# Kernel tuning notes

Hardware: AMD Instinct MI355X
Metric: run time of the kernel (lower is better)

## Reference

```python
import jax, jax.numpy as jnp
import numpy as np

N = 100000   # nodes
E = 400000   # edges (avg degree 4, NoC-mesh-like)
H = 512      # hidden_channels
F_IN = 1     # num_node_features


def _lin(key, fan_in, fan_out):
    # torch.nn.Linear default init: U(-1/sqrt(fan_in), 1/sqrt(fan_in))
    bound = 1.0 / np.sqrt(fan_in)
    return jax.random.uniform(key, (fan_in, fan_out), jnp.float32, -bound, bound)


def setup_inputs() -> dict:
    key = jax.random.key(0)
    ks = jax.random.split(key, 16)
    inp = {
        "x": jax.random.normal(ks[0], (N, F_IN), jnp.float32),
        "edge_index": jax.random.randint(ks[1], (2, E), 0, N, jnp.int32),
        # conv1: in=1 -> out=512
        "w_rel1": _lin(ks[2], F_IN, H),
        "b_rel1": jax.random.uniform(ks[3], (H,), jnp.float32, -1.0, 1.0),
        "w_root1": _lin(ks[4], F_IN, H),
        # conv2..4: 512 -> 512
        "w_rel2": _lin(ks[5], H, H),
        "b_rel2": jax.random.uniform(ks[6], (H,), jnp.float32, -1/np.sqrt(H), 1/np.sqrt(H)),
        "w_root2": _lin(ks[7], H, H),
        "w_rel3": _lin(ks[8], H, H),
        "b_rel3": jax.random.uniform(ks[9], (H,), jnp.float32, -1/np.sqrt(H), 1/np.sqrt(H)),
        "w_root3": _lin(ks[10], H, H),
        "w_rel4": _lin(ks[11], H, H),
        "b_rel4": jax.random.uniform(ks[12], (H,), jnp.float32, -1/np.sqrt(H), 1/np.sqrt(H)),
        "w_root4": _lin(ks[13], H, H),
    }
    return inp


def _graph_conv(x, src, dst, w_rel, b_rel, w_root):
    # PyG GraphConv (aggr='add'): out_i = W_rel @ sum_{j in N(i)} x_j + b_rel + W_root @ x_i
    # messages flow src (edge_index[0]) -> dst (edge_index[1])
    agg = jax.ops.segment_sum(x[src], dst, num_segments=N)  # [N, F_in]
    return agg @ w_rel + b_rel + x @ w_root


def reference(x, edge_index,
              w_rel1, b_rel1, w_root1,
              w_rel2, b_rel2, w_root2,
              w_rel3, b_rel3, w_root3,
              w_rel4, b_rel4, w_root4):
    src, dst = edge_index[0], edge_index[1]
    x1 = jax.nn.relu(_graph_conv(x,  src, dst, w_rel1, b_rel1, w_root1))
    x2 = jax.nn.relu(_graph_conv(x1, src, dst, w_rel2, b_rel2, w_root2)) + x1
    x3 = _graph_conv(x2, src, dst, w_rel3, b_rel3, w_root3) + x2
    x4 = _graph_conv(x3, src, dst, w_rel4, b_rel4, w_root4) + x3
    return x4
```

## Files before the change

kernel.cpp:

```cpp
#include <hip/hip_runtime.h>

#define NN 100000
#define EE 400000
#define HH 512
#define NB_SCAN 98

typedef __attribute__((ext_vector_type(8))) short short8;
typedef __attribute__((ext_vector_type(8))) unsigned short ushort8;
typedef __attribute__((ext_vector_type(4))) float f32x4;

__device__ inline unsigned short f2b(float f) {
    unsigned int u = __float_as_uint(f);
    return (unsigned short)((u + 0x7fffu + ((u >> 16) & 1u)) >> 16);
}
__device__ inline float b2f(unsigned short b) {
    return __uint_as_float(((unsigned int)b) << 16);
}

__global__ void histo_deg(const int* __restrict__ dst, int* __restrict__ deg) {
    int e = blockIdx.x * blockDim.x + threadIdx.x;
    if (e < EE) atomicAdd(&deg[dst[e]], 1);
}

__global__ void scan_reduce(const int* __restrict__ deg, int* __restrict__ blockSums) {
    __shared__ int s[256];
    int b = blockIdx.x, t = threadIdx.x;
    int base = b * 1024 + t * 4;
    int v = 0;
    #pragma unroll
    for (int j = 0; j < 4; ++j) { int i = base + j; if (i < NN) v += deg[i]; }
    s[t] = v; __syncthreads();
    for (int off = 128; off > 0; off >>= 1) {
        if (t < off) s[t] += s[t + off];
        __syncthreads();
    }
    if (t == 0) blockSums[b] = s[0];
}

__global__ void scan_top(int* __restrict__ blockSums, int* __restrict__ start) {
    __shared__ int s[128];
    int t = threadIdx.x;
    s[t] = (t < NB_SCAN) ? blockSums[t] : 0;
    __syncthreads();
    for (int off = 1; off < 128; off <<= 1) {
        int u = (t >= off) ? s[t - off] : 0;
        __syncthreads();
        s[t] += u;
        __syncthreads();
    }
    if (t < NB_SCAN) blockSums[t] = (t == 0) ? 0 : s[t - 1];
    if (t == 0) start[NN] = EE;
}

__global__ void scan_down(const int* __restrict__ deg, const int* __restrict__ blockSums,
                          int* __restrict__ start, int* __restrict__ cursor) {
    __shared__ int s[256];
    int b = blockIdx.x, t = threadIdx.x;
    int base = b * 1024 + t * 4;
    int v[4]; int sum = 0;
    #pragma unroll
    for (int j = 0; j < 4; ++j) {
        int i = base + j;
        v[j] = (i < NN) ? deg[i] : 0;
        sum += v[j];
    }
    s[t] = sum; __syncthreads();
    for (int off = 1; off < 256; off <<= 1) {
        int u = (t >= off) ? s[t - off] : 0;
        __syncthreads();
        s[t] += u;
        __syncthreads();
    }
    int excl = blockSums[b] + ((t == 0) ? 0 : s[t - 1]);
    #pragma unroll
    for (int j = 0; j < 4; ++j) {
        int i = base + j;
        if (i < NN) { start[i] = excl; cursor[i] = excl; excl += v[j]; }
    }
}

__global__ void csr_fill(const int* __restrict__ src, const int* __restrict__ dst,
                         int* __restrict__ cursor, int* __restrict__ eidx) {
    int e = blockIdx.x * blockDim.x + threadIdx.x;
    if (e < EE) {
        int p = atomicAdd(&cursor[dst[e]], 1);
        eidx[p] = src[e];
    }
}

__global__ void w_transpose(const float* __restrict__ w, unsigned short* __restrict__ wt) {
    int idx = blockIdx.x * 256 + threadIdx.x;
    int n = idx >> 9, k = idx & 511;
    wt[idx] = f2b(w[(size_t)k * HH + n]);
}

__global__ __launch_bounds__(256) void gather_rows_b(
    const unsigned short* __restrict__ xb, const int* __restrict__ start,
    const int* __restrict__ eidx, unsigned short* __restrict__ agg)
{
    int node = blockIdx.x * 4 + (threadIdx.x >> 6);
    if (node >= NN) return;
    int c0 = (threadIdx.x & 63) << 3;
    float a[8] = {0.f,0.f,0.f,0.f,0.f,0.f,0.f,0.f};
    int e0 = start[node], e1 = start[node + 1];
    int e = e0;
    for (; e + 4 <= e1; e += 4) {
        int s0 = eidx[e], s1 = eidx[e + 1], s2 = eidx[e + 2], s3 = eidx[e + 3];
        ushort8 v0 = *(const ushort8*)(xb + (size_t)s0 * HH + c0);
        ushort8 v1 = *(const ushort8*)(xb + (size_t)s1 * HH + c0);
        ushort8 v2 = *(const ushort8*)(xb + (size_t)s2 * HH + c0);
        ushort8 v3 = *(const ushort8*)(xb + (size_t)s3 * HH + c0);
        #pragma unroll
        for (int j = 0; j < 8; ++j)
            a[j] += (b2f(v0[j]) + b2f(v1[j])) + (b2f(v2[j]) + b2f(v3[j]));
    }
    for (; e < e1; ++e) {
        ushort8 v = *(const ushort8*)(xb + (size_t)eidx[e] * HH + c0);
        #pragma unroll
        for (int j = 0; j < 8; ++j) a[j] += b2f(v[j]);
    }
    ushort8 o;
    #pragma unroll
    for (int j = 0; j < 8; ++j) o[j] = f2b(a[j]);
    *(ushort8*)(agg + (size_t)node * HH + c0) = o;
}

__global__ void gather_scalar(const float* __restrict__ x, const int* __restrict__ start,
                              const int* __restrict__ eidx, float* __restrict__ agg0) {
    int i = blockIdx.x * blockDim.x + threadIdx.x;
    if (i >= NN) return;
    float s = 0.f;
    int e1 = start[i + 1];
    for (int e = start[i]; e < e1; ++e) s += x[eidx[e]];
    agg0[i] = s;
}

__global__ void layer1_expand(const float* __restrict__ x,
                              const float* __restrict__ agg0,
                              const float* __restrict__ w_rel,
                              const float* __restrict__ b,
                              const float* __restrict__ w_root,
                              unsigned short* __restrict__ x1b) {
    int idx = blockIdx.x * blockDim.x + threadIdx.x;
    int i = idx >> 7;
    if (i >= NN) return;
    int q = (idx & 127) << 2;
    float a = agg0[i], xv = x[i];
    float4 wr = *(const float4*)&w_rel[q];
    float4 bb = *(const float4*)&b[q];
    float4 wt = *(const float4*)&w_root[q];
    float4 o;
    o.x = fmaxf(fmaf(a, wr.x, fmaf(xv, wt.x, bb.x)), 0.f);
    o.y = fmaxf(fmaf(a, wr.y, fmaf(xv, wt.y, bb.y)), 0.f);
    o.z = fmaxf(fmaf(a, wr.z, fmaf(xv, wt.z, bb.z)), 0.f);
    o.w = fmaxf(fmaf(a, wr.w, fmaf(xv, wt.w, bb.w)), 0.f);
    ushort4 ob = { f2b(o.x), f2b(o.y), f2b(o.z), f2b(o.w) };
    *(ushort4*)&x1b[(size_t)i * HH + q] = ob;
}

__device__ inline void gload16(const void* g, void* l) {
    __builtin_amdgcn_global_load_lds(
        (const __attribute__((address_space(1))) unsigned int*)g,
        (__attribute__((address_space(3))) unsigned int*)l,
        16, 0, 0);
}

template<bool RELU, bool F32OUT>
__global__ __launch_bounds__(256, 4) void gemm_mfma(
    const unsigned short* __restrict__ AB, const unsigned short* __restrict__ XBp,
    const unsigned short* __restrict__ WrT, const unsigned short* __restrict__ WoT,
    const float* __restrict__ bias, const unsigned short* __restrict__ residb,
    float* __restrict__ out, unsigned short* __restrict__ outb)
{
    __shared__ unsigned short As[2 * 128 * 32];
    __shared__ unsigned short Bs[2 * 128 * 32];
    const int tid  = threadIdx.x;
    const int wave = tid >> 6, lane = tid & 63;

    const int bid = blockIdx.x;
    const int nid = (bid & 7) * 391 + (bid >> 3);
    const int col0 = (nid & 3) << 7;
    const int row0 = (nid >> 2) << 7;

    const int wr = wave >> 1, wc = wave & 1;
    const int l16 = lane & 15, lq = lane >> 4;
    const int sRow = lane >> 2;
    const int sColSwz = (((lane & 3) ^ ((lane >> 3) & 3)) << 3);
    const int xorslot = ((lq ^ ((lane >> 1) & 3)) << 3);

    int rowA[2], colB[2];
    #pragma unroll
    for (int i = 0; i < 2; ++i) {
        int chunk = (wave << 1) + i;
        int gr = row0 + chunk * 16 + sRow;
        rowA[i] = (gr >= NN) ? (NN - 1) : gr;
        colB[i] = col0 + chunk * 16 + sRow;
    }

    f32x4 acc[4][4];
    #pragma unroll
    for (int m = 0; m < 4; ++m)
        #pragma unroll
        for (int n = 0; n < 4; ++n)
            acc[m][n] = (f32x4){0.f, 0.f, 0.f, 0.f};

    auto STAGE = [&](unsigned short* Asb, unsigned short* Bsb, int t) {
        const int k0 = t << 5;
        const unsigned short* Ap = (k0 < 512) ? AB  : XBp;
        const unsigned short* Wp = (k0 < 512) ? WrT : WoT;
        const int kk = k0 & 511;
        #pragma unroll
        for (int i = 0; i < 2; ++i) {
            int chunk = (wave << 1) + i;
            gload16(Ap + (size_t)rowA[i] * HH + kk + sColSwz, Asb + chunk * 512);
            gload16(Wp + (size_t)colB[i] * HH + kk + sColSwz, Bsb + chunk * 512);
        }
    };

    auto COMPUTE = [&](const unsigned short* Asb, const unsigned short* Bsb) {
        short8 af[4], bfv[4];
        #pragma unroll
        for (int m = 0; m < 4; ++m)
            af[m] = *(const short8*)(Asb + (wr * 64 + m * 16 + l16) * 32 + xorslot);
        #pragma unroll
        for (int n = 0; n < 4; ++n)
            bfv[n] = *(const short8*)(Bsb + (wc * 64 + n * 16 + l16) * 32 + xorslot);
        #pragma unroll
        for (int m = 0; m < 4; ++m)
            #pragma unroll
            for (int n = 0; n < 4; ++n)
                acc[m][n] = __builtin_amdgcn_mfma_f32_16x16x32_bf16(af[m], bfv[n], acc[m][n], 0, 0, 0);
    };

    unsigned short* A0 = As;        unsigned short* A1 = As + 4096;
    unsigned short* B0 = Bs;        unsigned short* B1 = Bs + 4096;

    STAGE(A0, B0, 0);
    __syncthreads();
    #pragma unroll 1
    for (int t = 0; t < 32; t += 2) {
        STAGE(A1, B1, t + 1);
        COMPUTE(A0, B0);
        __syncthreads();
        if (t + 2 < 32) STAGE(A0, B0, t + 2);
        COMPUTE(A1, B1);
        __syncthreads();
    }

    float bias_n[4];
    #pragma unroll
    for (int n = 0; n < 4; ++n) bias_n[n] = bias[col0 + wc * 64 + n * 16 + l16];

    #pragma unroll
    for (int m = 0; m < 4; ++m) {
        #pragma unroll
        for (int j = 0; j < 4; ++j) {
            int row = row0 + wr * 64 + m * 16 + lq * 4 + j;
            if (row >= NN) continue;
            #pragma unroll
            for (int n = 0; n < 4; ++n) {
                int col = col0 + wc * 64 + n * 16 + l16;
                size_t off = (size_t)row * HH + col;
                float v = acc[m][n][j] + bias_n[n];
                if (RELU) v = fmaxf(v, 0.f);
                v += b2f(residb[off]);
                if (F32OUT) out[off] = v;
                else        outb[off] = f2b(v);
            }
        }
    }
}

extern "C" void kernel_launch(void* const* d_in, const int* in_sizes, int n_in,
                              void* d_out, int out_size, void* d_ws, size_t ws_size,
                              hipStream_t stream) {
    const float* x   = (const float*)d_in[0];
    const int*   ei  = (const int*)d_in[1];
    const int*   src = ei;
    const int*   dst = ei + EE;
    const float* w_rel1  = (const float*)d_in[2];
    const float* b_rel1  = (const float*)d_in[3];
    const float* w_root1 = (const float*)d_in[4];
    const float* w_rel2  = (const float*)d_in[5];
    const float* b_rel2  = (const float*)d_in[6];
    const float* w_root2 = (const float*)d_in[7];
    const float* w_rel3  = (const float*)d_in[8];
    const float* b_rel3  = (const float*)d_in[9];
    const float* w_root3 = (const float*)d_in[10];
    const float* w_rel4  = (const float*)d_in[11];
    const float* b_rel4  = (const float*)d_in[12];
    const float* w_root4 = (const float*)d_in[13];

    const size_t NH = (size_t)NN * HH;
    unsigned short* XB   = (unsigned short*)d_ws;
    unsigned short* XB2  = XB + NH;
    unsigned short* X3B  = XB2 + NH;
    unsigned short* AGB  = X3B + NH;
    unsigned short* WT   = AGB + NH;
    float*          agg0 = (float*)(WT + 6 * 262144);
    int*            csr  = (int*)(agg0 + NN);
    int* deg       = csr;
    int* start     = csr + NN;
    int* cursor    = start + NN + 1;
    int* eidx      = cursor + NN;
    int* blockSums = eidx + EE;
    float* out = (float*)d_out;

    unsigned short* WrT2 = WT;
    unsigned short* WoT2 = WT + 1 * 262144;
    unsigned short* WrT3 = WT + 2 * 262144;
    unsigned short* WoT3 = WT + 3 * 262144;
    unsigned short* WrT4 = WT + 4 * 262144;
    unsigned short* WoT4 = WT + 5 * 262144;

    const int gGemm = 3128;

    hipMemsetAsync(deg, 0, NN * sizeof(int), stream);
    histo_deg<<<(EE + 255) / 256, 256, 0, stream>>>(dst, deg);
    scan_reduce<<<NB_SCAN, 256, 0, stream>>>(deg, blockSums);
    scan_top<<<1, 128, 0, stream>>>(blockSums, start);
    scan_down<<<NB_SCAN, 256, 0, stream>>>(deg, blockSums, start, cursor);
    csr_fill<<<(EE + 255) / 256, 256, 0, stream>>>(src, dst, cursor, eidx);

    w_transpose<<<1024, 256, 0, stream>>>(w_rel2,  WrT2);
    w_transpose<<<1024, 256, 0, stream>>>(w_root2, WoT2);
    w_transpose<<<1024, 256, 0, stream>>>(w_rel3,  WrT3);
    w_transpose<<<1024, 256, 0, stream>>>(w_root3, WoT3);
    w_transpose<<<1024, 256, 0, stream>>>(w_rel4,  WrT4);
    w_transpose<<<1024, 256, 0, stream>>>(w_root4, WoT4);

    gather_scalar<<<(NN + 255) / 256, 256, 0, stream>>>(x, start, eidx, agg0);
    layer1_expand<<<50000, 256, 0, stream>>>(x, agg0, w_rel1, b_rel1, w_root1, XB);

    gather_rows_b<<<25000, 256, 0, stream>>>(XB, start, eidx, AGB);
    gemm_mfma<true, false><<<gGemm, 256, 0, stream>>>(
        AGB, XB, WrT2, WoT2, b_rel2, XB, nullptr, XB2);

    gather_rows_b<<<25000, 256, 0, stream>>>(XB2, start, eidx, AGB);
    gemm_mfma<false, false><<<gGemm, 256, 0, stream>>>(
        AGB, XB2, WrT3, WoT3, b_rel3, XB2, nullptr, X3B);

    gather_rows_b<<<25000, 256, 0, stream>>>(X3B, start, eidx, AGB);
    gemm_mfma<false, true><<<gGemm, 256, 0, stream>>>(
        AGB, X3B, WrT4, WoT4, b_rel4, X3B, out, nullptr);
}
```

Measured before the change: 810.6 us.

## Fold linear layers 3 and 4 into one GEMM via precomputed weight products

```diff
diff --git a/kernel.cpp b/kernel.cpp
--- a/kernel.cpp
+++ b/kernel.cpp
@@ -88,10 +88,31 @@
     }
 }
 
-__global__ void w_transpose(const float* __restrict__ w, unsigned short* __restrict__ wt) {
+__global__ void w_transpose(const float* __restrict__ w, unsigned short* __restrict__ wt, int addI) {
     int idx = blockIdx.x * 256 + threadIdx.x;
     int n = idx >> 9, k = idx & 511;
-    wt[idx] = f2b(w[(size_t)k * HH + n]);
+    float v = w[(size_t)k * HH + n] + ((addI && k == n) ? 1.f : 0.f);
+    wt[idx] = f2b(v);
+}
+__global__ void w_convert(const float* __restrict__ w, unsigned short* __restrict__ wb, int addI) {
+    int idx = blockIdx.x * 256 + threadIdx.x;
+    int k = idx >> 9, j = idx & 511;
+    float v = w[idx] + ((addI && k == j) ? 1.f : 0.f);
+    wb[idx] = f2b(v);
+}
+__global__ void cvec(const float* __restrict__ b3, const float* __restrict__ Wr4,
+                     const float* __restrict__ Wo4, const float* __restrict__ b4,
+                     float* __restrict__ c1, float* __restrict__ c2) {
+    int n = blockIdx.x * 256 + threadIdx.x;
+    if (n >= HH) return;
+    float a1 = 0.f, a2 = 0.f;
+    for (int j = 0; j < HH; ++j) {
+        float bj = b3[j];
+        a1 = fmaf(bj, Wr4[(size_t)j * HH + n], a1);
+        a2 = fmaf(bj, Wo4[(size_t)j * HH + n], a2);
+    }
+    c1[n] = a1;
+    c2[n] = a2 + b3[n] + b4[n];
 }
 
 __global__ __launch_bounds__(256) void gather_rows_b(
@@ -165,23 +186,20 @@
         16, 0, 0);
 }
 
-template<bool RELU, bool F32OUT>
-__global__ __launch_bounds__(256, 4) void gemm_mfma(
+__global__ __launch_bounds__(256, 3) void gemm_l2(
     const unsigned short* __restrict__ AB, const unsigned short* __restrict__ XBp,
     const unsigned short* __restrict__ WrT, const unsigned short* __restrict__ WoT,
     const float* __restrict__ bias, const unsigned short* __restrict__ residb,
-    float* __restrict__ out, unsigned short* __restrict__ outb)
+    unsigned short* __restrict__ outb)
 {
     __shared__ unsigned short As[2 * 128 * 32];
     __shared__ unsigned short Bs[2 * 128 * 32];
     const int tid  = threadIdx.x;
     const int wave = tid >> 6, lane = tid & 63;
-
     const int bid = blockIdx.x;
     const int nid = (bid & 7) * 391 + (bid >> 3);
     const int col0 = (nid & 3) << 7;
     const int row0 = (nid >> 2) << 7;
-
     const int wr = wave >> 1, wc = wave & 1;
     const int l16 = lane & 15, lq = lane >> 4;
     const int sRow = lane >> 2;
@@ -201,8 +219,7 @@
     #pragma unroll
     for (int m = 0; m < 4; ++m)
         #pragma unroll
-        for (int n = 0; n < 4; ++n)
-            acc[m][n] = (f32x4){0.f, 0.f, 0.f, 0.f};
+        for (int n = 0; n < 4; ++n) acc[m][n] = (f32x4){0.f,0.f,0.f,0.f};
 
     auto STAGE = [&](unsigned short* Asb, unsigned short* Bsb, int t) {
         const int k0 = t << 5;
@@ -216,7 +233,6 @@
             gload16(Wp + (size_t)colB[i] * HH + kk + sColSwz, Bsb + chunk * 512);
         }
     };
-
     auto COMPUTE = [&](const unsigned short* Asb, const unsigned short* Bsb) {
         short8 af[4], bfv[4];
         #pragma unroll
@@ -232,9 +248,7 @@
                 acc[m][n] = __builtin_amdgcn_mfma_f32_16x16x32_bf16(af[m], bfv[n], acc[m][n], 0, 0, 0);
     };
 
-    unsigned short* A0 = As;        unsigned short* A1 = As + 4096;
-    unsigned short* B0 = Bs;        unsigned short* B1 = Bs + 4096;
-
+    unsigned short *A0 = As, *A1 = As + 4096, *B0 = Bs, *B1 = Bs + 4096;
     STAGE(A0, B0, 0);
     __syncthreads();
     #pragma unroll 1
@@ -250,7 +264,6 @@
     float bias_n[4];
     #pragma unroll
     for (int n = 0; n < 4; ++n) bias_n[n] = bias[col0 + wc * 64 + n * 16 + l16];
-
     #pragma unroll
     for (int m = 0; m < 4; ++m) {
         #pragma unroll
@@ -261,14 +274,196 @@
             for (int n = 0; n < 4; ++n) {
                 int col = col0 + wc * 64 + n * 16 + l16;
                 size_t off = (size_t)row * HH + col;
-                float v = acc[m][n][j] + bias_n[n];
-                if (RELU) v = fmaxf(v, 0.f);
-                v += b2f(residb[off]);
-                if (F32OUT) out[off] = v;
-                else        outb[off] = f2b(v);
+                float v = fmaxf(acc[m][n][j] + bias_n[n], 0.f) + b2f(residb[off]);
+                outb[off] = f2b(v);
             }
         }
     }
+}
+
+__global__ __launch_bounds__(256, 3) void gemm_f34(
+    const unsigned short* __restrict__ G2, const unsigned short* __restrict__ G1,
+    const unsigned short* __restrict__ X2,
+    const unsigned short* __restrict__ P1T, const unsigned short* __restrict__ P2T,
+    const unsigned short* __restrict__ P3T,
+    const float* __restrict__ c1, const float* __restrict__ c2,
+    const int* __restrict__ deg, float* __restrict__ out)
+{
+    __shared__ unsigned short As[2 * 128 * 32];
+    __shared__ unsigned short Bs[2 * 128 * 32];
+    const int tid  = threadIdx.x;
+    const int wave = tid >> 6, lane = tid & 63;
+    const int bid = blockIdx.x;
+    const int nid = (bid & 7) * 391 + (bid >> 3);
+    const int col0 = (nid & 3) << 7;
+    const int row0 = (nid >> 2) << 7;
+    const int wr = wave >> 1, wc = wave & 1;
+    const int l16 = lane & 15, lq = lane >> 4;
+    const int sRow = lane >> 2;
+    const int sColSwz = (((lane & 3) ^ ((lane >> 3) & 3)) << 3);
+    const int xorslot = ((lq ^ ((lane >> 1) & 3)) << 3);
+
+    int rowA[2], colB[2];
+    #pragma unroll
+    for (int i = 0; i < 2; ++i) {
+        int chunk = (wave << 1) + i;
+        int gr = row0 + chunk * 16 + sRow;
+        rowA[i] = (gr >= NN) ? (NN - 1) : gr;
+        colB[i] = col0 + chunk * 16 + sRow;
+    }
+
+    f32x4 acc[4][4];
+    #pragma unroll
+    for (int m = 0; m < 4; ++m)
+        #pragma unroll
+        for (int n = 0; n < 4; ++n) acc[m][n] = (f32x4){0.f,0.f,0.f,0.f};
+
+    auto STAGE = [&](unsigned short* Asb, unsigned short* Bsb, int t) {
+        const int s = t >> 4;
+        const unsigned short* Ap = (s == 0) ? G2  : ((s == 1) ? G1  : X2);
+        const unsigned short* Wp = (s == 0) ? P1T : ((s == 1) ? P2T : P3T);
+        const int kk = (t & 15) << 5;
+        #pragma unroll
+        for (int i = 0; i < 2; ++i) {
+            int chunk = (wave << 1) + i;
+            gload16(Ap + (size_t)rowA[i] * HH + kk + sColSwz, Asb + chunk * 512);
+            gload16(Wp + (size_t)colB[i] * HH + kk + sColSwz, Bsb + chunk * 512);
+        }
+    };
+    auto COMPUTE = [&](const unsigned short* Asb, const unsigned short* Bsb) {
+        short8 af[4], bfv[4];
+        #pragma unroll
+        for (int m = 0; m < 4; ++m)
+            af[m] = *(const short8*)(Asb + (wr * 64 + m * 16 + l16) * 32 + xorslot);
+        #pragma unroll
+        for (int n = 0; n < 4; ++n)
+            bfv[n] = *(const short8*)(Bsb + (wc * 64 + n * 16 + l16) * 32 + xorslot);
+        #pragma unroll
+        for (int m = 0; m < 4; ++m)
+            #pragma unroll
+            for (int n = 0; n < 4; ++n)
+                acc[m][n] = __builtin_amdgcn_mfma_f32_16x16x32_bf16(af[m], bfv[n], acc[m][n], 0, 0, 0);
+    };
+
+    unsigned short *A0 = As, *A1 = As + 4096, *B0 = Bs, *B1 = Bs + 4096;
+    STAGE(A0, B0, 0);
+    __syncthreads();
+    #pragma unroll 1
+    for (int t = 0; t < 48; t += 2) {
+        STAGE(A1, B1, t + 1);
+        COMPUTE(A0, B0);
+        __syncthreads();
+        if (t + 2 < 48) STAGE(A0, B0, t + 2);
+        COMPUTE(A1, B1);
+        __syncthreads();
+    }
+
+    float c1_n[4], c2_n[4];
+    #pragma unroll
+    for (int n = 0; n < 4; ++n) {
+        int col = col0 + wc * 64 + n * 16 + l16;
+        c1_n[n] = c1[col];
+        c2_n[n] = c2[col];
+    }
+    #pragma unroll
+    for (int m = 0; m < 4; ++m) {
+        #pragma unroll
+        for (int j = 0; j < 4; ++j) {
+            int row = row0 + wr * 64 + m * 16 + lq * 4 + j;
+            if (row >= NN) continue;
+            float dg = (float)deg[row];
+            #pragma unroll
+            for (int n = 0; n < 4; ++n) {
+                int col = col0 + wc * 64 + n * 16 + l16;
+                out[(size_t)row * HH + col] = acc[m][n][j] + dg * c1_n[n] + c2_n[n];
+            }
+        }
+    }
+}
+
+template<int NSRC>
+__global__ __launch_bounds__(256) void gemm_cmp(
+    const unsigned short* __restrict__ A0p, const unsigned short* __restrict__ W0p,
+    const unsigned short* __restrict__ A1p, const unsigned short* __restrict__ W1p,
+    unsigned short* __restrict__ outb)
+{
+    __shared__ unsigned short As[2 * 128 * 32];
+    __shared__ unsigned short Bs[2 * 128 * 32];
+    const int tid  = threadIdx.x;
+    const int wave = tid >> 6, lane = tid & 63;
+    const int col0 = (blockIdx.x & 3) << 7;
+    const int row0 = (blockIdx.x >> 2) << 7;
+    const int wr = wave >> 1, wc = wave & 1;
+    const int l16 = lane & 15, lq = lane >> 4;
+    const int sRow = lane >> 2;
+    const int sColSwz = (((lane & 3) ^ ((lane >> 3) & 3)) << 3);
+    const int xorslot = ((lq ^ ((lane >> 1) & 3)) << 3);
+
+    int rowA[2], colB[2];
+    #pragma unroll
+    for (int i = 0; i < 2; ++i) {
+        int chunk = (wave << 1) + i;
+        rowA[i] = row0 + chunk * 16 + sRow;
+        colB[i] = col0 + chunk * 16 + sRow;
+    }
+
+    f32x4 acc[4][4];
+    #pragma unroll
+    for (int m = 0; m < 4; ++m)
+        #pragma unroll
+        for (int n = 0; n < 4; ++n) acc[m][n] = (f32x4){0.f,0.f,0.f,0.f};
+
+    auto STAGE = [&](unsigned short* Asb, unsigned short* Bsb, int t) {
+        const unsigned short* Ap = (NSRC == 1 || t < 16) ? A0p : A1p;
+        const unsigned short* Wp = (NSRC == 1 || t < 16) ? W0p : W1p;
+        const int kk = (t & 15) << 5;
+        #pragma unroll
+        for (int i = 0; i < 2; ++i) {
+            int chunk = (wave << 1) + i;
+            gload16(Ap + (size_t)rowA[i] * HH + kk + sColSwz, Asb + chunk * 512);
+            gload16(Wp + (size_t)colB[i] * HH + kk + sColSwz, Bsb + chunk * 512);
+        }
+    };
+    auto COMPUTE = [&](const unsigned short* Asb, const unsigned short* Bsb) {
+        short8 af[4], bfv[4];
+        #pragma unroll
+        for (int m = 0; m < 4; ++m)
+            af[m] = *(const short8*)(Asb + (wr * 64 + m * 16 + l16) * 32 + xorslot);
+        #pragma unroll
+        for (int n = 0; n < 4; ++n)
+            bfv[n] = *(const short8*)(Bsb + (wc * 64 + n * 16 + l16) * 32 + xorslot);
+        #pragma unroll
+        for (int m = 0; m < 4; ++m)
+            #pragma unroll
+            for (int n = 0; n < 4; ++n)
+                acc[m][n] = __builtin_amdgcn_mfma_f32_16x16x32_bf16(af[m], bfv[n], acc[m][n], 0, 0, 0);
+    };
+
+    const int NT = NSRC * 16;
+    unsigned short *A0 = As, *A1 = As + 4096, *B0 = Bs, *B1 = Bs + 4096;
+    STAGE(A0, B0, 0);
+    __syncthreads();
+    #pragma unroll 1
+    for (int t = 0; t < NT; t += 2) {
+        STAGE(A1, B1, t + 1);
+        COMPUTE(A0, B0);
+        __syncthreads();
+        if (t + 2 < NT) STAGE(A0, B0, t + 2);
+        COMPUTE(A1, B1);
+        __syncthreads();
+    }
+
+    #pragma unroll
+    for (int m = 0; m < 4; ++m)
+        #pragma unroll
+        for (int j = 0; j < 4; ++j) {
+            int row = row0 + wr * 64 + m * 16 + lq * 4 + j;
+            #pragma unroll
+            for (int n = 0; n < 4; ++n) {
+                int col = col0 + wc * 64 + n * 16 + l16;
+                outb[(size_t)row * HH + col] = f2b(acc[m][n][j]);
+            }
+        }
 }
 
 extern "C" void kernel_launch(void* const* d_in, const int* in_sizes, int n_in,
@@ -292,13 +487,25 @@
     const float* w_root4 = (const float*)d_in[13];
 
     const size_t NH = (size_t)NN * HH;
+    const size_t WSZ = 262144;
     unsigned short* XB   = (unsigned short*)d_ws;
     unsigned short* XB2  = XB + NH;
-    unsigned short* X3B  = XB2 + NH;
-    unsigned short* AGB  = X3B + NH;
-    unsigned short* WT   = AGB + NH;
-    float*          agg0 = (float*)(WT + 6 * 262144);
-    int*            csr  = (int*)(agg0 + NN);
+    unsigned short* AGB  = XB2 + NH;
+    unsigned short* AGB2 = AGB + NH;
+    unsigned short* WT   = AGB2 + NH;
+    unsigned short* WrT2 = WT;
+    unsigned short* WoT2 = WT + 1 * WSZ;
+    unsigned short* WrT4 = WT + 2 * WSZ;
+    unsigned short* M4T  = WT + 3 * WSZ;
+    unsigned short* Wr3b = WT + 4 * WSZ;
+    unsigned short* M3b  = WT + 5 * WSZ;
+    unsigned short* P1T  = WT + 6 * WSZ;
+    unsigned short* P2T  = WT + 7 * WSZ;
+    unsigned short* P3T  = WT + 8 * WSZ;
+    float* c1   = (float*)(WT + 9 * WSZ);
+    float* c2   = c1 + HH;
+    float* agg0 = c2 + HH;
+    int*   csr  = (int*)(agg0 + NN);
     int* deg       = csr;
     int* start     = csr + NN;
     int* cursor    = start + NN + 1;
@@ -306,13 +513,6 @@
     int* blockSums = eidx + EE;
     float* out = (float*)d_out;
 
-    unsigned short* WrT2 = WT;
-    unsigned short* WoT2 = WT + 1 * 262144;
-    unsigned short* WrT3 = WT + 2 * 262144;
-    unsigned short* WoT3 = WT + 3 * 262144;
-    unsigned short* WrT4 = WT + 4 * 262144;
-    unsigned short* WoT4 = WT + 5 * 262144;
-
     const int gGemm = 3128;
 
     hipMemsetAsync(deg, 0, NN * sizeof(int), stream);
@@ -322,25 +522,24 @@
     scan_down<<<NB_SCAN, 256, 0, stream>>>(deg, blockSums, start, cursor);
     csr_fill<<<(EE + 255) / 256, 256, 0, stream>>>(src, dst, cursor, eidx);
 
-    w_transpose<<<1024, 256, 0, stream>>>(w_rel2,  WrT2);
-    w_transpose<<<1024, 256, 0, stream>>>(w_root2, WoT2);
-    w_transpose<<<1024, 256, 0, stream>>>(w_rel3,  WrT3);
-    w_transpose<<<1024, 256, 0, stream>>>(w_root3, WoT3);
-    w_transpose<<<1024, 256, 0, stream>>>(w_rel4,  WrT4);
-    w_transpose<<<1024, 256, 0, stream>>>(w_root4, WoT4);
+    w_transpose<<<1024, 256, 0, stream>>>(w_rel2,  WrT2, 0);
+    w_transpose<<<1024, 256, 0, stream>>>(w_root2, WoT2, 0);
+    w_transpose<<<1024, 256, 0, stream>>>(w_rel4,  WrT4, 0);
+    w_transpose<<<1024, 256, 0, stream>>>(w_root4, M4T,  1);
+    w_convert <<<1024, 256, 0, stream>>>(w_rel3,  Wr3b, 0);
+    w_convert <<<1024, 256, 0, stream>>>(w_root3, M3b,  1);
+    gemm_cmp<1><<<16, 256, 0, stream>>>(WrT4, Wr3b, nullptr, nullptr, P1T);
+    gemm_cmp<2><<<16, 256, 0, stream>>>(WrT4, M3b,  M4T, Wr3b,       P2T);
+    gemm_cmp<1><<<16, 256, 0, stream>>>(M4T,  M3b,  nullptr, nullptr, P3T);
+    cvec<<<2, 256, 0, stream>>>(b_rel3, w_rel4, w_root4, b_rel4, c1, c2);
 
     gather_scalar<<<(NN + 255) / 256, 256, 0, stream>>>(x, start, eidx, agg0);
     layer1_expand<<<50000, 256, 0, stream>>>(x, agg0, w_rel1, b_rel1, w_root1, XB);
 
     gather_rows_b<<<25000, 256, 0, stream>>>(XB, start, eidx, AGB);
-    gemm_mfma<true, false><<<gGemm, 256, 0, stream>>>(
-        AGB, XB, WrT2, WoT2, b_rel2, XB, nullptr, XB2);
+    gemm_l2<<<gGemm, 256, 0, stream>>>(AGB, XB, WrT2, WoT2, b_rel2, XB, XB2);
 
     gather_rows_b<<<25000, 256, 0, stream>>>(XB2, start, eidx, AGB);
-    gemm_mfma<false, false><<<gGemm, 256, 0, stream>>>(
-        AGB, XB2, WrT3, WoT3, b_rel3, XB2, nullptr, X3B);
-
-    gather_rows_b<<<25000, 256, 0, stream>>>(X3B, start, eidx, AGB);
-    gemm_mfma<false, true><<<gGemm, 256, 0, stream>>>(
-        AGB, X3B, WrT4, WoT4, b_rel4, X3B, out, nullptr);
-}
+    gather_rows_b<<<25000, 256, 0, stream>>>(AGB, start, eidx, AGB2);
+    gemm_f34<<<gGemm, 256, 0, stream>>>(AGB2, AGB, XB2, P1T, P2T, P3T, c1, c2, deg, out);
+}
```

New measurement: 982.6 us. 21.2% more time.
